# Optimization experiments

Hardware: AMD Instinct MI355X
Metric: run time of the kernel (lower is better)

## Reference

```python
import jax, jax.numpy as jnp
import numpy as np

P_DIM, L_DIM, D, O = 1100, 1024, 1024, 1024  # protein/label embed dims, latent, mlp width
B, NL = 16, 5000  # num_sequences, num_labels


def setup_inputs() -> dict:
    key = jax.random.key(0)
    ks = jax.random.split(key, 10)
    s = 0.02
    return {
        "sequence_embeddings": jax.random.normal(ks[0], (B, P_DIM), jnp.float32),
        "label_embeddings": jax.random.normal(ks[1], (NL, L_DIM), jnp.float32),
        "Wp": jax.random.normal(ks[2], (D, P_DIM), jnp.float32) * s,  # W_p (no bias)
        "Wl": jax.random.normal(ks[3], (D, L_DIM), jnp.float32) * s,  # W_l (no bias)
        "W1": jax.random.normal(ks[4], (O, 2 * D), jnp.float32) * s,  # Linear(2D -> O)
        "b1": jnp.zeros((O,), jnp.float32),
        "W2": jax.random.normal(ks[5], (O, O), jnp.float32) * s,      # Linear(O -> O)
        "b2": jnp.zeros((O,), jnp.float32),
        "W3": jax.random.normal(ks[6], (1, O), jnp.float32) * s,      # Linear(O -> 1)
        "b3": jnp.zeros((1,), jnp.float32),
    }


def reference(sequence_embeddings, label_embeddings, Wp, Wl, W1, b1, W2, b2, W3, b3):
    # Latent projections
    P_e = sequence_embeddings @ Wp.T           # [B, D]
    L_e = label_embeddings @ Wl.T              # [NL, D]
    # First MLP layer on concat([P_e, L_e]) over the cross join, computed by
    # splitting W1 into its P and L halves and broadcast-summing (same math as
    # cat + Linear, avoids materializing the [B*NL, 2D] concat).
    hp = P_e @ W1[:, :D].T                     # [B, O]
    hl = L_e @ W1[:, D:].T                     # [NL, O]
    h = jax.nn.relu(hp[:, None, :] + hl[None, :, :] + b1)   # [B, NL, O]
    h = jax.nn.relu(h @ W2.T + b2)             # [B, NL, O]
    logits = (h @ W3.T + b3)[..., 0]           # [B, NL]
    return logits
```

## Files before the change

kernel.cpp:

```cpp
#include <hip/hip_runtime.h>
#include <hip/hip_bf16.h>
#include <stdint.h>

typedef __bf16 bf16;
typedef __bf16 bf16x4 __attribute__((ext_vector_type(4)));
typedef __bf16 bf16x8 __attribute__((ext_vector_type(8)));
typedef float floatx4 __attribute__((ext_vector_type(4)));

#define B_SEQ 16
#define NLBL  5000
#define DLAT  1024
#define PDIM  1100
#define NROWS (B_SEQ * NLBL)

__device__ __forceinline__ void gload_lds16(const bf16* g, bf16* l) {
    __builtin_amdgcn_global_load_lds(
        (const __attribute__((address_space(1))) void*)g,
        (__attribute__((address_space(3))) void*)l, 16, 0, 0);
}

__device__ __forceinline__ bf16x8 cvt8(const float* s) {
    floatx4 a = *(const floatx4*)s;
    floatx4 b = *(const floatx4*)(s + 4);
    bf16x8 o;
    o[0] = (bf16)a.x; o[1] = (bf16)a.y; o[2] = (bf16)a.z; o[3] = (bf16)a.w;
    o[4] = (bf16)b.x; o[5] = (bf16)b.y; o[6] = (bf16)b.z; o[7] = (bf16)b.w;
    return o;
}

__device__ __forceinline__ void barx() {
    asm volatile("" ::: "memory");
    __builtin_amdgcn_s_barrier();
    asm volatile("" ::: "memory");
}

#define PSEG_M    256
#define PSEG_LAB  2756
#define PSEG_W2   3268
#define PSEG_PE   3524
#define PSEG_END  3837

__global__ __launch_bounds__(256)
void prep_kernel(const float* __restrict__ label, bf16* __restrict__ label_b,
                 const float* __restrict__ W2, bf16* __restrict__ W2_b,
                 const float* __restrict__ W1, const float* __restrict__ Wl,
                 bf16* __restrict__ M_bf,
                 const float* __restrict__ seq, const float* __restrict__ Wp,
                 float* __restrict__ Pe,
                 float* __restrict__ out, const float* __restrict__ b3) {
    __shared__ bf16 MAs[64 * 72];
    __shared__ bf16 MBs[64 * 72];
    const int blk = blockIdx.x;
    const int t = threadIdx.x;

    if (blk < PSEG_M) {
        const int m0 = (blk >> 4) * 64;
        const int n0g = (blk & 15) * 64;
        const int wave = t >> 6, lane = t & 63;
        const int wm = (wave & 1) * 32, wn = (wave >> 1) * 32;
        const int lm = lane & 15, quad = lane >> 4;
        const int a_r = t >> 2, a_c = (t & 3) * 16;
        const int b_kr = t >> 4, b_l = (t & 15) * 4;
        floatx4 acc[2][2] = {};

        for (int k0 = 0; k0 < 1024; k0 += 64) {
            const float* ap = W1 + (size_t)(m0 + a_r) * 2048 + 1024 + k0 + a_c;
            *(bf16x8*)(MAs + a_r * 72 + a_c) = cvt8(ap);
            *(bf16x8*)(MAs + a_r * 72 + a_c + 8) = cvt8(ap + 8);
#pragma unroll
            for (int ps = 0; ps < 4; ++ps) {
                int kr = b_kr + ps * 16;
                floatx4 v = *(const floatx4*)(Wl + (size_t)(k0 + kr) * 1024 + n0g + b_l);
                MBs[(b_l + 0) * 72 + kr] = (bf16)v.x;
                MBs[(b_l + 1) * 72 + kr] = (bf16)v.y;
                MBs[(b_l + 2) * 72 + kr] = (bf16)v.z;
                MBs[(b_l + 3) * 72 + kr] = (bf16)v.w;
            }
            __syncthreads();
#pragma unroll
            for (int ks = 0; ks < 2; ++ks) {
                bf16x8 af[2], bg[2];
#pragma unroll
                for (int mi = 0; mi < 2; ++mi)
                    af[mi] = *(const bf16x8*)(MAs + (wm + mi * 16 + lm) * 72 + ks * 32 + quad * 8);
#pragma unroll
                for (int ni = 0; ni < 2; ++ni)
                    bg[ni] = *(const bf16x8*)(MBs + (wn + ni * 16 + lm) * 72 + ks * 32 + quad * 8);
#pragma unroll
                for (int mi = 0; mi < 2; ++mi)
#pragma unroll
                    for (int ni = 0; ni < 2; ++ni)
                        acc[mi][ni] = __builtin_amdgcn_mfma_f32_16x16x32_bf16(af[mi], bg[ni], acc[mi][ni], 0, 0, 0);
            }
            __syncthreads();
        }
#pragma unroll
        for (int mi = 0; mi < 2; ++mi)
#pragma unroll
            for (int r = 0; r < 4; ++r)
#pragma unroll
                for (int ni = 0; ni < 2; ++ni)
                    M_bf[(size_t)(m0 + wm + mi * 16 + quad * 4 + r) * 1024 + n0g + wn + ni * 16 + lm] =
                        (bf16)acc[mi][ni][r];
    } else if (blk < PSEG_LAB) {
        int i = (blk - PSEG_M) * 256 + t;
        ((bf16x8*)label_b)[i] = cvt8(label + (size_t)i * 8);
    } else if (blk < PSEG_W2) {
        int i = (blk - PSEG_LAB) * 256 + t;
        ((bf16x8*)W2_b)[i] = cvt8(W2 + (size_t)i * 8);
    } else if (blk < PSEG_PE) {
        int w = (blk - PSEG_W2) * 4 + (t >> 6);
        int l = t & 63;
        floatx4 wv[5];
#pragma unroll
        for (int k = 0; k < 5; ++k) {
            int g = l + 64 * k;
            wv[k] = (g < 275) ? *(const floatx4*)(Wp + (size_t)w * PDIM + g * 4)
                              : floatx4{0.f, 0.f, 0.f, 0.f};
        }
        for (int b = 0; b < B_SEQ; ++b) {
            float acc = 0.f;
#pragma unroll
            for (int k = 0; k < 5; ++k) {
                int g = l + 64 * k;
                if (g < 275) {
                    floatx4 sv = *(const floatx4*)(seq + (size_t)b * PDIM + g * 4);
                    acc += wv[k].x * sv.x + wv[k].y * sv.y + wv[k].z * sv.z + wv[k].w * sv.w;
                }
            }
#pragma unroll
            for (int off = 32; off; off >>= 1) acc += __shfl_xor(acc, off, 64);
            if (l == 0) Pe[b * DLAT + w] = acc;
        }
    } else {
        int i = (blk - PSEG_PE) * 256 + t;
        if (i < NROWS) out[i] = b3[0];
    }
}


__global__ __launch_bounds__(256)
void hpb_kernel(const float* __restrict__ Pe, const float* __restrict__ W1,
                const float* __restrict__ b1, float* __restrict__ hpb) {
    int w = blockIdx.x * 4 + (threadIdx.x >> 6);
    int l = threadIdx.x & 63;
    floatx4 wv[4];
#pragma unroll
    for (int k = 0; k < 4; ++k)
        wv[k] = *(const floatx4*)(W1 + (size_t)w * 2048 + (l + 64 * k) * 4);
    for (int b = 0; b < B_SEQ; ++b) {
        float acc = 0.f;
#pragma unroll
        for (int k = 0; k < 4; ++k) {
            floatx4 pv = *(const floatx4*)(Pe + (size_t)b * DLAT + (l + 64 * k) * 4);
            acc += wv[k].x * pv.x + wv[k].y * pv.y + wv[k].z * pv.z + wv[k].w * pv.w;
        }
#pragma unroll
        for (int off = 32; off; off >>= 1) acc += __shfl_xor(acc, off, 64);
        if (l == 0) hpb[b * DLAT + w] = acc + b1[w];
    }
}


__global__ __launch_bounds__(256)
void hl_h1_kernel(const bf16* __restrict__ A, const bf16* __restrict__ Bt,
                  const float* __restrict__ hpb, bf16* __restrict__ h1) {
    __shared__ __align__(16) char smem[25600];
    bf16* As = (bf16*)smem;
    bf16* Bs = (bf16*)(smem + 8192);
    bf16* Ls = (bf16*)smem;
    float* hpbs = (float*)(smem + 17408);

    const int t = threadIdx.x;
    const int d0 = blockIdx.x * 128;
    const int n0 = blockIdx.y * 64;
    const int wave = t >> 6, lane = t & 63;
    const int wm = (wave & 1) * 32;
    const int wn = (wave >> 1) * 64;
    const int lm = lane & 15, quad = lane >> 4;
    const int sw = lm & 7;
    const int srow = t >> 3;
    const int scg0 = t & 7;
    const int sbase = (t & 192) * 8;

    floatx4 acc[2][4] = {};

    for (int k0 = 0; k0 < 1024; k0 += 64) {
#pragma unroll
        for (int p = 0; p < 2; ++p) {
            int row = p * 32 + srow;
            int cg = scg0 ^ (row & 7);
            int grow = n0 + row; if (grow >= NLBL) grow = NLBL - 1;
            gload_lds16(A + (size_t)grow * 1024 + k0 + cg * 8, As + p * 2048 + sbase);
        }
#pragma unroll
        for (int p = 0; p < 4; ++p) {
            int row = p * 32 + srow;
            int cg = scg0 ^ (row & 7);
            gload_lds16(Bt + (size_t)(d0 + row) * 1024 + k0 + cg * 8, Bs + p * 2048 + sbase);
        }
        __syncthreads();
#pragma unroll
        for (int k = 0; k < 64; k += 32) {
            bf16x8 af[2], bg[4];
            int ko = (((k >> 3) + quad) ^ sw) * 8;
#pragma unroll
            for (int mi = 0; mi < 2; ++mi)
                af[mi] = *(const bf16x8*)(As + (wm + mi * 16 + lm) * 64 + ko);
#pragma unroll
            for (int ni = 0; ni < 4; ++ni)
                bg[ni] = *(const bf16x8*)(Bs + (wn + ni * 16 + lm) * 64 + ko);
#pragma unroll
            for (int mi = 0; mi < 2; ++mi)
#pragma unroll
                for (int ni = 0; ni < 4; ++ni)
                    acc[mi][ni] = __builtin_amdgcn_mfma_f32_16x16x32_bf16(af[mi], bg[ni], acc[mi][ni], 0, 0, 0);
        }
        __syncthreads();
    }

#pragma unroll
    for (int mi = 0; mi < 2; ++mi)
#pragma unroll
        for (int r = 0; r < 4; ++r)
#pragma unroll
            for (int ni = 0; ni < 4; ++ni)
                Ls[(wm + mi * 16 + quad * 4 + r) * 136 + wn + ni * 16 + lm] =
                    (bf16)acc[mi][ni][r];
    {
        int dl = (t & 31) * 4;
        int b = t >> 5;
        *(floatx4*)(hpbs + b * 128 + dl) =
            *(const floatx4*)(hpb + (size_t)b * DLAT + d0 + dl);
        *(floatx4*)(hpbs + (b + 8) * 128 + dl) =
            *(const floatx4*)(hpb + (size_t)(b + 8) * DLAT + d0 + dl);
    }
    __syncthreads();

    const int g = t & 15;
    const int r0 = t >> 4;
    bf16x8 hlv[4];
#pragma unroll
    for (int p = 0; p < 4; ++p)
        hlv[p] = *(const bf16x8*)(Ls + (p * 16 + r0) * 136 + g * 8);

    for (int b = 0; b < B_SEQ; ++b) {
        floatx4 h0 = *(const floatx4*)(hpbs + b * 128 + g * 8);
        floatx4 h4 = *(const floatx4*)(hpbs + b * 128 + g * 8 + 4);
        size_t rowbase = (size_t)b * NLBL * 1024;
#pragma unroll
        for (int p = 0; p < 4; ++p) {
            int n = n0 + p * 16 + r0;
            if (n >= NLBL) continue;
            bf16x8 o;
            o[0] = (bf16)fmaxf((float)hlv[p][0] + h0.x, 0.f);
            o[1] = (bf16)fmaxf((float)hlv[p][1] + h0.y, 0.f);
            o[2] = (bf16)fmaxf((float)hlv[p][2] + h0.z, 0.f);
            o[3] = (bf16)fmaxf((float)hlv[p][3] + h0.w, 0.f);
            o[4] = (bf16)fmaxf((float)hlv[p][4] + h4.x, 0.f);
            o[5] = (bf16)fmaxf((float)hlv[p][5] + h4.y, 0.f);
            o[6] = (bf16)fmaxf((float)hlv[p][6] + h4.z, 0.f);
            o[7] = (bf16)fmaxf((float)hlv[p][7] + h4.w, 0.f);
            *(bf16x8*)(h1 + rowbase + (size_t)n * 1024 + d0 + g * 8) = o;
        }
    }
}


__device__ __forceinline__ void stage_A256(const bf16* __restrict__ src, bf16* dst,
                                           int m0, int kc, int t) {
#pragma unroll
    for (int i = 0; i < 4; ++i) {
        int s = t + i * 512;
        int row = s >> 3;
        int cg = (s & 7) ^ (row & 7);
        int grow = m0 + row;
        if (grow >= NROWS) grow = NROWS - 1;
        gload_lds16(src + (size_t)grow * 1024 + kc + cg * 8, dst + s * 8);
    }
}

__device__ __forceinline__ void stage_B256(const bf16* __restrict__ src, bf16* dst,
                                           int n0, int kc, int t) {
#pragma unroll
    for (int i = 0; i < 4; ++i) {
        int s = t + i * 512;
        int row = s >> 3;
        int cg = (s & 7) ^ (row & 7);
        gload_lds16(src + (size_t)(n0 + row) * 1024 + kc + cg * 8, dst + s * 8);
    }
}

__global__ __launch_bounds__(512, 2)
void gemm_h2(const bf16* __restrict__ h1, const bf16* __restrict__ W2b,
             const float* __restrict__ b2, const float* __restrict__ W3,
             float* __restrict__ out) {
    __shared__ bf16 As[32768];
    __shared__ bf16 Bs[32768];
    const int t = threadIdx.x;

    int orig = blockIdx.x;
    int xcd = orig & 7, idx = orig >> 3;
    int wg = (xcd < 4 ? xcd * 157 : 628 + (xcd - 4) * 156) + idx;
    const int mt = wg >> 2, nt = wg & 3;
    const int m0 = mt * 256, n0 = nt * 256;

    const int wave = t >> 6, lane = t & 63;
    const int wr = wave >> 2, wc = wave & 3;
    const int wrow = wr * 128, wcol = wc * 64;
    const int lm = lane & 15, quad = lane >> 4;
    const int swz = lm & 7;

    floatx4 acc[8][4] = {};

    stage_A256(h1, As, m0, 0, t);
    stage_B256(W2b, Bs, n0, 0, t);
    asm volatile("s_waitcnt vmcnt(0)" ::: "memory");
    barx();

    for (int kt = 0; kt < 16; ++kt) {
        const int db = kt & 1;
        const bf16* Ad = As + db * 16384;
        const bf16* Bd = Bs + db * 16384;
        bf16* An = As + (db ^ 1) * 16384;
        bf16* Bn = Bs + (db ^ 1) * 16384;
        const bool pf = (kt < 15);
        const int kc = (kt + 1) * 64;

        bf16x8 a[4][2], blo[2][2], bhi[2][2];

#pragma unroll
        for (int mi = 0; mi < 4; ++mi) {
            const bf16* rp = Ad + (wrow + mi * 16 + lm) * 64;
            a[mi][0] = *(const bf16x8*)(rp + ((quad ^ swz) << 3));
            a[mi][1] = *(const bf16x8*)(rp + (((4 + quad) ^ swz) << 3));
        }
#pragma unroll
        for (int ni = 0; ni < 2; ++ni) {
            const bf16* rp = Bd + (wcol + ni * 16 + lm) * 64;
            blo[ni][0] = *(const bf16x8*)(rp + ((quad ^ swz) << 3));
            blo[ni][1] = *(const bf16x8*)(rp + (((4 + quad) ^ swz) << 3));
        }
        if (pf) stage_A256(h1, An, m0, kc, t);
        barx();
        __builtin_amdgcn_s_setprio(1);
#pragma unroll
        for (int mi = 0; mi < 4; ++mi)
#pragma unroll
            for (int ni = 0; ni < 2; ++ni) {
                acc[mi][ni] = __builtin_amdgcn_mfma_f32_16x16x32_bf16(a[mi][0], blo[ni][0], acc[mi][ni], 0, 0, 0);
                acc[mi][ni] = __builtin_amdgcn_mfma_f32_16x16x32_bf16(a[mi][1], blo[ni][1], acc[mi][ni], 0, 0, 0);
            }
        __builtin_amdgcn_s_setprio(0);
        barx();

#pragma unroll
        for (int ni = 0; ni < 2; ++ni) {
            const bf16* rp = Bd + (wcol + 32 + ni * 16 + lm) * 64;
            bhi[ni][0] = *(const bf16x8*)(rp + ((quad ^ swz) << 3));
            bhi[ni][1] = *(const bf16x8*)(rp + (((4 + quad) ^ swz) << 3));
        }
        if (pf) stage_B256(W2b, Bn, n0, kc, t);
        barx();
        __builtin_amdgcn_s_setprio(1);
#pragma unroll
        for (int mi = 0; mi < 4; ++mi)
#pragma unroll
            for (int ni = 0; ni < 2; ++ni) {
                acc[mi][2 + ni] = __builtin_amdgcn_mfma_f32_16x16x32_bf16(a[mi][0], bhi[ni][0], acc[mi][2 + ni], 0, 0, 0);
                acc[mi][2 + ni] = __builtin_amdgcn_mfma_f32_16x16x32_bf16(a[mi][1], bhi[ni][1], acc[mi][2 + ni], 0, 0, 0);
            }
        __builtin_amdgcn_s_setprio(0);
        barx();

#pragma unroll
        for (int mi = 0; mi < 4; ++mi) {
            const bf16* rp = Ad + (wrow + 64 + mi * 16 + lm) * 64;
            a[mi][0] = *(const bf16x8*)(rp + ((quad ^ swz) << 3));
            a[mi][1] = *(const bf16x8*)(rp + (((4 + quad) ^ swz) << 3));
        }
        barx();
        __builtin_amdgcn_s_setprio(1);
#pragma unroll
        for (int mi = 0; mi < 4; ++mi)
#pragma unroll
            for (int ni = 0; ni < 2; ++ni) {
                acc[4 + mi][2 + ni] = __builtin_amdgcn_mfma_f32_16x16x32_bf16(a[mi][0], bhi[ni][0], acc[4 + mi][2 + ni], 0, 0, 0);
                acc[4 + mi][2 + ni] = __builtin_amdgcn_mfma_f32_16x16x32_bf16(a[mi][1], bhi[ni][1], acc[4 + mi][2 + ni], 0, 0, 0);
            }
        __builtin_amdgcn_s_setprio(0);
        barx();

        __builtin_amdgcn_s_setprio(1);
#pragma unroll
        for (int mi = 0; mi < 4; ++mi)
#pragma unroll
            for (int ni = 0; ni < 2; ++ni) {
                acc[4 + mi][ni] = __builtin_amdgcn_mfma_f32_16x16x32_bf16(a[mi][0], blo[ni][0], acc[4 + mi][ni], 0, 0, 0);
                acc[4 + mi][ni] = __builtin_amdgcn_mfma_f32_16x16x32_bf16(a[mi][1], blo[ni][1], acc[4 + mi][ni], 0, 0, 0);
            }
        __builtin_amdgcn_s_setprio(0);
        asm volatile("s_waitcnt vmcnt(0)" ::: "memory");
        barx();
    }

    float w3v[4], b2v[4];
#pragma unroll
    for (int ni = 0; ni < 4; ++ni) {
        int col = n0 + wcol + ni * 16 + lm;
        w3v[ni] = W3[col];
        b2v[ni] = b2[col];
    }
#pragma unroll
    for (int mi = 0; mi < 8; ++mi) {
#pragma unroll
        for (int r = 0; r < 4; ++r) {
            float sacc = 0.f;
#pragma unroll
            for (int ni = 0; ni < 4; ++ni)
                sacc += fmaxf(acc[mi][ni][r] + b2v[ni], 0.f) * w3v[ni];
            sacc += __shfl_xor(sacc, 1, 64);
            sacc += __shfl_xor(sacc, 2, 64);
            sacc += __shfl_xor(sacc, 4, 64);
            sacc += __shfl_xor(sacc, 8, 64);
            int row = m0 + wrow + mi * 16 + quad * 4 + r;
            if (lm == 0 && row < NROWS)
                atomicAdd(out + row, sacc);
        }
    }
}


extern "C" void kernel_launch(void* const* d_in, const int* in_sizes, int n_in,
                              void* d_out, int out_size, void* d_ws, size_t ws_size,
                              hipStream_t stream) {
    const float* seq   = (const float*)d_in[0];
    const float* label = (const float*)d_in[1];
    const float* Wp    = (const float*)d_in[2];
    const float* Wl    = (const float*)d_in[3];
    const float* W1    = (const float*)d_in[4];
    const float* b1    = (const float*)d_in[5];
    const float* W2    = (const float*)d_in[6];
    const float* b2    = (const float*)d_in[7];
    const float* W3    = (const float*)d_in[8];
    const float* b3    = (const float*)d_in[9];
    float* out = (float*)d_out;
    (void)n_in; (void)in_sizes; (void)out_size; (void)ws_size;

    size_t off = 0;
    auto alloc = [&](size_t bytes) {
        void* p = (char*)d_ws + off;
        off += (bytes + 255) & ~(size_t)255;
        return p;
    };
    bf16* label_b = (bf16*)alloc((size_t)NLBL * 1024 * 2);
    bf16* W2_b    = (bf16*)alloc((size_t)1024 * 1024 * 2);
    bf16* M_bf    = (bf16*)alloc((size_t)1024 * 1024 * 2);
    float* Pe     = (float*)alloc((size_t)B_SEQ * 1024 * 4);
    float* hpb    = (float*)alloc((size_t)B_SEQ * 1024 * 4);
    bf16* h1      = (bf16*)alloc((size_t)NROWS * 1024 * 2);

    prep_kernel<<<PSEG_END, 256, 0, stream>>>(label, label_b, W2, W2_b, W1, Wl,
                                              M_bf, seq, Wp, Pe, out, b3);
    hpb_kernel<<<256, 256, 0, stream>>>(Pe, W1, b1, hpb);
    hl_h1_kernel<<<dim3(8, 79), 256, 0, stream>>>(label_b, M_bf, hpb, h1);
    gemm_h2<<<1252, 512, 0, stream>>>(h1, W2_b, b2, W3, out);
}
```

Before: 325.8 us.

## Fuse broadcast-add ReLU into the second GEMM's A-tile staging

Stops materializing the full [B*NL,1024] bf16 h1 tensor. hl is now stored once as fp32 [NL,1024], and the h2 GEMM builds each A tile on the fly as relu(hl + hpb[b]) in registers before writing it to LDS. The grid is remapped to (label tile, batch, column tile), giving 1280 blocks. This removes a large global write and read, but the A-tile staging now goes through registers, costs VALU conversion work inside the main loop, and reads hl again for every batch index, which relies on cache reuse.

New measurement: 392.6 us. +20.5%, slower.

```diff
diff --git a/kernel.cpp b/kernel.cpp
--- a/kernel.cpp
+++ b/kernel.cpp
@@ -163,13 +163,11 @@
 
 
 __global__ __launch_bounds__(256)
-void hl_h1_kernel(const bf16* __restrict__ A, const bf16* __restrict__ Bt,
-                  const float* __restrict__ hpb, bf16* __restrict__ h1) {
-    __shared__ __align__(16) char smem[25600];
+void hl_kernel(const bf16* __restrict__ A, const bf16* __restrict__ Bt,
+               float* __restrict__ hl) {
+    __shared__ __align__(16) char smem[24576];
     bf16* As = (bf16*)smem;
     bf16* Bs = (bf16*)(smem + 8192);
-    bf16* Ls = (bf16*)smem;
-    float* hpbs = (float*)(smem + 17408);
 
     const int t = threadIdx.x;
     const int d0 = blockIdx.x * 128;
@@ -222,63 +220,15 @@
 #pragma unroll
     for (int mi = 0; mi < 2; ++mi)
 #pragma unroll
-        for (int r = 0; r < 4; ++r)
+        for (int r = 0; r < 4; ++r) {
+            int n = n0 + wm + mi * 16 + quad * 4 + r;
+            if (n >= NLBL) continue;
 #pragma unroll
             for (int ni = 0; ni < 4; ++ni)
-                Ls[(wm + mi * 16 + quad * 4 + r) * 136 + wn + ni * 16 + lm] =
-                    (bf16)acc[mi][ni][r];
-    {
-        int dl = (t & 31) * 4;
-        int b = t >> 5;
-        *(floatx4*)(hpbs + b * 128 + dl) =
-            *(const floatx4*)(hpb + (size_t)b * DLAT + d0 + dl);
-        *(floatx4*)(hpbs + (b + 8) * 128 + dl) =
-            *(const floatx4*)(hpb + (size_t)(b + 8) * DLAT + d0 + dl);
-    }
-    __syncthreads();
-
-    const int g = t & 15;
-    const int r0 = t >> 4;
-    bf16x8 hlv[4];
-#pragma unroll
-    for (int p = 0; p < 4; ++p)
-        hlv[p] = *(const bf16x8*)(Ls + (p * 16 + r0) * 136 + g * 8);
-
-    for (int b = 0; b < B_SEQ; ++b) {
-        floatx4 h0 = *(const floatx4*)(hpbs + b * 128 + g * 8);
-        floatx4 h4 = *(const floatx4*)(hpbs + b * 128 + g * 8 + 4);
-        size_t rowbase = (size_t)b * NLBL * 1024;
-#pragma unroll
-        for (int p = 0; p < 4; ++p) {
-            int n = n0 + p * 16 + r0;
-            if (n >= NLBL) continue;
-            bf16x8 o;
-            o[0] = (bf16)fmaxf((float)hlv[p][0] + h0.x, 0.f);
-            o[1] = (bf16)fmaxf((float)hlv[p][1] + h0.y, 0.f);
-            o[2] = (bf16)fmaxf((float)hlv[p][2] + h0.z, 0.f);
-            o[3] = (bf16)fmaxf((float)hlv[p][3] + h0.w, 0.f);
-            o[4] = (bf16)fmaxf((float)hlv[p][4] + h4.x, 0.f);
-            o[5] = (bf16)fmaxf((float)hlv[p][5] + h4.y, 0.f);
-            o[6] = (bf16)fmaxf((float)hlv[p][6] + h4.z, 0.f);
-            o[7] = (bf16)fmaxf((float)hlv[p][7] + h4.w, 0.f);
-            *(bf16x8*)(h1 + rowbase + (size_t)n * 1024 + d0 + g * 8) = o;
-        }
-    }
-}
-
-
-__device__ __forceinline__ void stage_A256(const bf16* __restrict__ src, bf16* dst,
-                                           int m0, int kc, int t) {
-#pragma unroll
-    for (int i = 0; i < 4; ++i) {
-        int s = t + i * 512;
-        int row = s >> 3;
-        int cg = (s & 7) ^ (row & 7);
-        int grow = m0 + row;
-        if (grow >= NROWS) grow = NROWS - 1;
-        gload_lds16(src + (size_t)grow * 1024 + kc + cg * 8, dst + s * 8);
-    }
-}
+                hl[(size_t)n * 1024 + d0 + wn + ni * 16 + lm] = acc[mi][ni][r];
+        }
+}
+
 
 __device__ __forceinline__ void stage_B256(const bf16* __restrict__ src, bf16* dst,
                                            int n0, int kc, int t) {
@@ -292,18 +242,22 @@
 }
 
 __global__ __launch_bounds__(512, 2)
-void gemm_h2(const bf16* __restrict__ h1, const bf16* __restrict__ W2b,
-             const float* __restrict__ b2, const float* __restrict__ W3,
-             float* __restrict__ out) {
+void gemm_fused(const float* __restrict__ hl, const float* __restrict__ hpb,
+                const bf16* __restrict__ W2b, const float* __restrict__ b2,
+                const float* __restrict__ W3, float* __restrict__ out) {
     __shared__ bf16 As[32768];
     __shared__ bf16 Bs[32768];
+    __shared__ float hpbs[1024];
     const int t = threadIdx.x;
 
     int orig = blockIdx.x;
-    int xcd = orig & 7, idx = orig >> 3;
-    int wg = (xcd < 4 ? xcd * 157 : 628 + (xcd - 4) * 156) + idx;
-    const int mt = wg >> 2, nt = wg & 3;
-    const int m0 = mt * 256, n0 = nt * 256;
+    int wg = (orig & 7) * 160 + (orig >> 3);
+    const int ct = wg & 3;
+    const int pairidx = wg >> 2;
+    const int nt = pairidx >> 4;
+    const int b = pairidx & 15;
+    const int m0 = nt * 256;
+    const int n0 = ct * 256;
 
     const int wave = t >> 6, lane = t & 63;
     const int wr = wave >> 2, wc = wave & 3;
@@ -311,11 +265,43 @@
     const int lm = lane & 15, quad = lane >> 4;
     const int swz = lm & 7;
 
+    const int rbase = t >> 3;
+    const int g = t & 7;
+    const int sw8 = (g ^ (rbase & 7)) << 3;
+
     floatx4 acc[8][4] = {};
-
-    stage_A256(h1, As, m0, 0, t);
+    floatx4 hv[4][2];
+
+    if (t < 256)
+        ((floatx4*)hpbs)[t] = ((const floatx4*)(hpb + (size_t)b * 1024))[t];
     stage_B256(W2b, Bs, n0, 0, t);
-    asm volatile("s_waitcnt vmcnt(0)" ::: "memory");
+#pragma unroll
+    for (int i = 0; i < 4; ++i) {
+        int grow = m0 + rbase + i * 64; if (grow > NLBL - 1) grow = NLBL - 1;
+        const float* p = hl + (size_t)grow * 1024 + g * 8;
+        hv[i][0] = *(const floatx4*)p;
+        hv[i][1] = *(const floatx4*)(p + 4);
+    }
+    asm volatile("s_waitcnt lgkmcnt(0)" ::: "memory");
+    barx();
+    {
+        floatx4 hp0 = *(const floatx4*)(hpbs + g * 8);
+        floatx4 hp1 = *(const floatx4*)(hpbs + g * 8 + 4);
+#pragma unroll
+        for (int i = 0; i < 4; ++i) {
+            bf16x8 o;
+            o[0] = (bf16)fmaxf(hv[i][0].x + hp0.x, 0.f);
+            o[1] = (bf16)fmaxf(hv[i][0].y + hp0.y, 0.f);
+            o[2] = (bf16)fmaxf(hv[i][0].z + hp0.z, 0.f);
+            o[3] = (bf16)fmaxf(hv[i][0].w + hp0.w, 0.f);
+            o[4] = (bf16)fmaxf(hv[i][1].x + hp1.x, 0.f);
+            o[5] = (bf16)fmaxf(hv[i][1].y + hp1.y, 0.f);
+            o[6] = (bf16)fmaxf(hv[i][1].z + hp1.z, 0.f);
+            o[7] = (bf16)fmaxf(hv[i][1].w + hp1.w, 0.f);
+            *(bf16x8*)(As + (rbase + i * 64) * 64 + sw8) = o;
+        }
+    }
+    asm volatile("s_waitcnt vmcnt(0) lgkmcnt(0)" ::: "memory");
     barx();
 
     for (int kt = 0; kt < 16; ++kt) {
@@ -328,6 +314,7 @@
         const int kc = (kt + 1) * 64;
 
         bf16x8 a[4][2], blo[2][2], bhi[2][2];
+        floatx4 hp0, hp1;
 
 #pragma unroll
         for (int mi = 0; mi < 4; ++mi) {
@@ -341,7 +328,16 @@
             blo[ni][0] = *(const bf16x8*)(rp + ((quad ^ swz) << 3));
             blo[ni][1] = *(const bf16x8*)(rp + (((4 + quad) ^ swz) << 3));
         }
-        if (pf) stage_A256(h1, An, m0, kc, t);
+        if (pf) {
+#pragma unroll
+            for (int i = 0; i < 4; ++i) {
+                int grow = m0 + rbase + i * 64; if (grow > NLBL - 1) grow = NLBL - 1;
+                const float* p = hl + (size_t)grow * 1024 + kc + g * 8;
+                hv[i][0] = *(const floatx4*)p;
+                hv[i][1] = *(const floatx4*)(p + 4);
+            }
+            stage_B256(W2b, Bn, n0, kc, t);
+        }
         barx();
         __builtin_amdgcn_s_setprio(1);
 #pragma unroll
@@ -360,7 +356,6 @@
             bhi[ni][0] = *(const bf16x8*)(rp + ((quad ^ swz) << 3));
             bhi[ni][1] = *(const bf16x8*)(rp + (((4 + quad) ^ swz) << 3));
         }
-        if (pf) stage_B256(W2b, Bn, n0, kc, t);
         barx();
         __builtin_amdgcn_s_setprio(1);
 #pragma unroll
@@ -379,6 +374,10 @@
             a[mi][0] = *(const bf16x8*)(rp + ((quad ^ swz) << 3));
             a[mi][1] = *(const bf16x8*)(rp + (((4 + quad) ^ swz) << 3));
         }
+        if (pf) {
+            hp0 = *(const floatx4*)(hpbs + kc + g * 8);
+            hp1 = *(const floatx4*)(hpbs + kc + g * 8 + 4);
+        }
         barx();
         __builtin_amdgcn_s_setprio(1);
 #pragma unroll
@@ -391,6 +390,21 @@
         __builtin_amdgcn_s_setprio(0);
         barx();
 
+        if (pf) {
+#pragma unroll
+            for (int i = 0; i < 4; ++i) {
+                bf16x8 o;
+                o[0] = (bf16)fmaxf(hv[i][0].x + hp0.x, 0.f);
+                o[1] = (bf16)fmaxf(hv[i][0].y + hp0.y, 0.f);
+                o[2] = (bf16)fmaxf(hv[i][0].z + hp0.z, 0.f);
+                o[3] = (bf16)fmaxf(hv[i][0].w + hp0.w, 0.f);
+                o[4] = (bf16)fmaxf(hv[i][1].x + hp1.x, 0.f);
+                o[5] = (bf16)fmaxf(hv[i][1].y + hp1.y, 0.f);
+                o[6] = (bf16)fmaxf(hv[i][1].z + hp1.z, 0.f);
+                o[7] = (bf16)fmaxf(hv[i][1].w + hp1.w, 0.f);
+                *(bf16x8*)(An + (rbase + i * 64) * 64 + sw8) = o;
+            }
+        }
         __builtin_amdgcn_s_setprio(1);
 #pragma unroll
         for (int mi = 0; mi < 4; ++mi)
@@ -400,7 +414,7 @@
                 acc[4 + mi][ni] = __builtin_amdgcn_mfma_f32_16x16x32_bf16(a[mi][1], blo[ni][1], acc[4 + mi][ni], 0, 0, 0);
             }
         __builtin_amdgcn_s_setprio(0);
-        asm volatile("s_waitcnt vmcnt(0)" ::: "memory");
+        asm volatile("s_waitcnt vmcnt(0) lgkmcnt(0)" ::: "memory");
         barx();
     }
 
@@ -423,9 +437,9 @@
             sacc += __shfl_xor(sacc, 2, 64);
             sacc += __shfl_xor(sacc, 4, 64);
             sacc += __shfl_xor(sacc, 8, 64);
-            int row = m0 + wrow + mi * 16 + quad * 4 + r;
-            if (lm == 0 && row < NROWS)
-                atomicAdd(out + row, sacc);
+            int nrow = m0 + wrow + mi * 16 + quad * 4 + r;
+            if (lm == 0 && nrow < NLBL)
+                atomicAdd(out + (size_t)b * NLBL + nrow, sacc);
         }
     }
 }
@@ -458,11 +472,11 @@
     bf16* M_bf    = (bf16*)alloc((size_t)1024 * 1024 * 2);
     float* Pe     = (float*)alloc((size_t)B_SEQ * 1024 * 4);
     float* hpb    = (float*)alloc((size_t)B_SEQ * 1024 * 4);
-    bf16* h1      = (bf16*)alloc((size_t)NROWS * 1024 * 2);
+    float* hl     = (float*)alloc((size_t)NLBL * 1024 * 4);
 
     prep_kernel<<<PSEG_END, 256, 0, stream>>>(label, label_b, W2, W2_b, W1, Wl,
                                               M_bf, seq, Wp, Pe, out, b3);
     hpb_kernel<<<256, 256, 0, stream>>>(Pe, W1, b1, hpb);
-    hl_h1_kernel<<<dim3(8, 79), 256, 0, stream>>>(label_b, M_bf, hpb, h1);
-    gemm_h2<<<1252, 512, 0, stream>>>(h1, W2_b, b2, W3, out);
-}
+    hl_kernel<<<dim3(8, 79), 256, 0, stream>>>(label_b, M_bf, hl);
+    gemm_fused<<<1280, 512, 0, stream>>>(hl, hpb, W2_b, b2, W3, out);
+}
```

## Prefetch next-tile LDS fragments into registers during last MFMA quadrant

Applied to the files above, without the earlier changes.

Restructures the gemm_h2 main loop so the first A/B fragments of the next k-tile are read from LDS into registers during the final MFMA quadrant of the current tile. The quadrant order and the points where the global->LDS stages are issued are also rearranged, and the MFMA loops now run k-slice outermost. The goal is to hide LDS read latency behind matrix math across iterations. In exchange it holds more live fragment registers, which could raise VGPR pressure or cause spills.

Result: slower. 348.8 us (+7.1%).

```diff
diff --git a/kernel.cpp b/kernel.cpp
--- a/kernel.cpp
+++ b/kernel.cpp
@@ -310,97 +310,113 @@
     const int wrow = wr * 128, wcol = wc * 64;
     const int lm = lane & 15, quad = lane >> 4;
     const int swz = lm & 7;
+    const int sl0 = (quad ^ swz) << 3;
+    const int sl1 = ((4 + quad) ^ swz) << 3;
 
     floatx4 acc[8][4] = {};
+    bf16x8 aLo[4][2], aHi[4][2], bLo[2][2], bHi[2][2];
 
     stage_A256(h1, As, m0, 0, t);
     stage_B256(W2b, Bs, n0, 0, t);
     asm volatile("s_waitcnt vmcnt(0)" ::: "memory");
     barx();
+#pragma unroll
+    for (int mi = 0; mi < 4; ++mi) {
+        const bf16* rp = As + (wrow + mi * 16 + lm) * 64;
+        aLo[mi][0] = *(const bf16x8*)(rp + sl0);
+        aLo[mi][1] = *(const bf16x8*)(rp + sl1);
+    }
+#pragma unroll
+    for (int ni = 0; ni < 2; ++ni) {
+        const bf16* rp = Bs + (wcol + ni * 16 + lm) * 64;
+        bLo[ni][0] = *(const bf16x8*)(rp + sl0);
+        bLo[ni][1] = *(const bf16x8*)(rp + sl1);
+    }
 
     for (int kt = 0; kt < 16; ++kt) {
         const int db = kt & 1;
         const bf16* Ad = As + db * 16384;
         const bf16* Bd = Bs + db * 16384;
+        const bf16* Anr = As + (db ^ 1) * 16384;
+        const bf16* Bnr = Bs + (db ^ 1) * 16384;
         bf16* An = As + (db ^ 1) * 16384;
         bf16* Bn = Bs + (db ^ 1) * 16384;
         const bool pf = (kt < 15);
         const int kc = (kt + 1) * 64;
 
-        bf16x8 a[4][2], blo[2][2], bhi[2][2];
-
-#pragma unroll
-        for (int mi = 0; mi < 4; ++mi) {
-            const bf16* rp = Ad + (wrow + mi * 16 + lm) * 64;
-            a[mi][0] = *(const bf16x8*)(rp + ((quad ^ swz) << 3));
-            a[mi][1] = *(const bf16x8*)(rp + (((4 + quad) ^ swz) << 3));
-        }
-#pragma unroll
-        for (int ni = 0; ni < 2; ++ni) {
-            const bf16* rp = Bd + (wcol + ni * 16 + lm) * 64;
-            blo[ni][0] = *(const bf16x8*)(rp + ((quad ^ swz) << 3));
-            blo[ni][1] = *(const bf16x8*)(rp + (((4 + quad) ^ swz) << 3));
-        }
-        if (pf) stage_A256(h1, An, m0, kc, t);
-        barx();
-        __builtin_amdgcn_s_setprio(1);
-#pragma unroll
-        for (int mi = 0; mi < 4; ++mi)
-#pragma unroll
-            for (int ni = 0; ni < 2; ++ni) {
-                acc[mi][ni] = __builtin_amdgcn_mfma_f32_16x16x32_bf16(a[mi][0], blo[ni][0], acc[mi][ni], 0, 0, 0);
-                acc[mi][ni] = __builtin_amdgcn_mfma_f32_16x16x32_bf16(a[mi][1], blo[ni][1], acc[mi][ni], 0, 0, 0);
-            }
-        __builtin_amdgcn_s_setprio(0);
-        barx();
-
 #pragma unroll
         for (int ni = 0; ni < 2; ++ni) {
             const bf16* rp = Bd + (wcol + 32 + ni * 16 + lm) * 64;
-            bhi[ni][0] = *(const bf16x8*)(rp + ((quad ^ swz) << 3));
-            bhi[ni][1] = *(const bf16x8*)(rp + (((4 + quad) ^ swz) << 3));
-        }
-        if (pf) stage_B256(W2b, Bn, n0, kc, t);
+            bHi[ni][0] = *(const bf16x8*)(rp + sl0);
+            bHi[ni][1] = *(const bf16x8*)(rp + sl1);
+        }
+        if (pf) stage_A256(h1, An, m0, kc, t);
         barx();
         __builtin_amdgcn_s_setprio(1);
 #pragma unroll
-        for (int mi = 0; mi < 4; ++mi)
-#pragma unroll
-            for (int ni = 0; ni < 2; ++ni) {
-                acc[mi][2 + ni] = __builtin_amdgcn_mfma_f32_16x16x32_bf16(a[mi][0], bhi[ni][0], acc[mi][2 + ni], 0, 0, 0);
-                acc[mi][2 + ni] = __builtin_amdgcn_mfma_f32_16x16x32_bf16(a[mi][1], bhi[ni][1], acc[mi][2 + ni], 0, 0, 0);
-            }
+        for (int ks = 0; ks < 2; ++ks)
+#pragma unroll
+            for (int mi = 0; mi < 4; ++mi)
+#pragma unroll
+                for (int ni = 0; ni < 2; ++ni)
+                    acc[mi][ni] = __builtin_amdgcn_mfma_f32_16x16x32_bf16(aLo[mi][ks], bLo[ni][ks], acc[mi][ni], 0, 0, 0);
         __builtin_amdgcn_s_setprio(0);
         barx();
 
 #pragma unroll
         for (int mi = 0; mi < 4; ++mi) {
             const bf16* rp = Ad + (wrow + 64 + mi * 16 + lm) * 64;
-            a[mi][0] = *(const bf16x8*)(rp + ((quad ^ swz) << 3));
-            a[mi][1] = *(const bf16x8*)(rp + (((4 + quad) ^ swz) << 3));
-        }
+            aHi[mi][0] = *(const bf16x8*)(rp + sl0);
+            aHi[mi][1] = *(const bf16x8*)(rp + sl1);
+        }
+        if (pf) stage_B256(W2b, Bn, n0, kc, t);
         barx();
         __builtin_amdgcn_s_setprio(1);
 #pragma unroll
-        for (int mi = 0; mi < 4; ++mi)
-#pragma unroll
-            for (int ni = 0; ni < 2; ++ni) {
-                acc[4 + mi][2 + ni] = __builtin_amdgcn_mfma_f32_16x16x32_bf16(a[mi][0], bhi[ni][0], acc[4 + mi][2 + ni], 0, 0, 0);
-                acc[4 + mi][2 + ni] = __builtin_amdgcn_mfma_f32_16x16x32_bf16(a[mi][1], bhi[ni][1], acc[4 + mi][2 + ni], 0, 0, 0);
-            }
+        for (int ks = 0; ks < 2; ++ks)
+#pragma unroll
+            for (int mi = 0; mi < 4; ++mi)
+#pragma unroll
+                for (int ni = 0; ni < 2; ++ni)
+                    acc[mi][2 + ni] = __builtin_amdgcn_mfma_f32_16x16x32_bf16(aLo[mi][ks], bHi[ni][ks], acc[mi][2 + ni], 0, 0, 0);
         __builtin_amdgcn_s_setprio(0);
         barx();
 
         __builtin_amdgcn_s_setprio(1);
 #pragma unroll
-        for (int mi = 0; mi < 4; ++mi)
-#pragma unroll
-            for (int ni = 0; ni < 2; ++ni) {
-                acc[4 + mi][ni] = __builtin_amdgcn_mfma_f32_16x16x32_bf16(a[mi][0], blo[ni][0], acc[4 + mi][ni], 0, 0, 0);
-                acc[4 + mi][ni] = __builtin_amdgcn_mfma_f32_16x16x32_bf16(a[mi][1], blo[ni][1], acc[4 + mi][ni], 0, 0, 0);
-            }
+        for (int ks = 0; ks < 2; ++ks)
+#pragma unroll
+            for (int mi = 0; mi < 4; ++mi)
+#pragma unroll
+                for (int ni = 0; ni < 2; ++ni)
+                    acc[4 + mi][ni] = __builtin_amdgcn_mfma_f32_16x16x32_bf16(aHi[mi][ks], bLo[ni][ks], acc[4 + mi][ni], 0, 0, 0);
         __builtin_amdgcn_s_setprio(0);
         asm volatile("s_waitcnt vmcnt(0)" ::: "memory");
+        barx();
+
+        if (pf) {
+#pragma unroll
+            for (int mi = 0; mi < 4; ++mi) {
+                const bf16* rp = Anr + (wrow + mi * 16 + lm) * 64;
+                aLo[mi][0] = *(const bf16x8*)(rp + sl0);
+                aLo[mi][1] = *(const bf16x8*)(rp + sl1);
+            }
+#pragma unroll
+            for (int ni = 0; ni < 2; ++ni) {
+                const bf16* rp = Bnr + (wcol + ni * 16 + lm) * 64;
+                bLo[ni][0] = *(const bf16x8*)(rp + sl0);
+                bLo[ni][1] = *(const bf16x8*)(rp + sl1);
+            }
+        }
+        __builtin_amdgcn_s_setprio(1);
+#pragma unroll
+        for (int ks = 0; ks < 2; ++ks)
+#pragma unroll
+            for (int mi = 0; mi < 4; ++mi)
+#pragma unroll
+                for (int ni = 0; ni < 2; ++ni)
+                    acc[4 + mi][2 + ni] = __builtin_amdgcn_mfma_f32_16x16x32_bf16(aHi[mi][ks], bHi[ni][ks], acc[4 + mi][2 + ni], 0, 0, 0);
+        __builtin_amdgcn_s_setprio(0);
         barx();
     }
 
```
